# Performance work log

Measured on AMD Instinct MI355X. Metric: run time of the kernel, lower is better.

The kernel has to match this reference:

```python
import jax, jax.numpy as jnp
import numpy as np
import math

HIDDEN = 1024
HEADS = 16
HEAD_DIM = HIDDEN // HEADS
B, S = 2, 2048


def setup_inputs() -> dict:
    key = jax.random.key(0)
    ks = jax.random.split(key, 10)
    std = 1.0 / math.sqrt(HIDDEN)
    mk = lambda k: (jax.random.normal(k, (HIDDEN, HIDDEN), jnp.float32) * std)
    return {
        "hidden_states": jax.random.normal(ks[0], (B, S, HIDDEN), jnp.float32),
        "attention_mask": jnp.zeros((B, 1, 1, S), jnp.float32),
        "wq": mk(ks[1]), "bq": jnp.zeros((HIDDEN,), jnp.float32),
        "wk": mk(ks[2]), "bk": jnp.zeros((HIDDEN,), jnp.float32),
        "wv": mk(ks[3]), "bv": jnp.zeros((HIDDEN,), jnp.float32),
        "wo": mk(ks[4]), "bo": jnp.zeros((HIDDEN,), jnp.float32),
    }


def reference(hidden_states, attention_mask, wq, bq, wk, bk, wv, bv, wo, bo):
    b, s, _ = hidden_states.shape
    scale = math.sqrt(HEAD_DIM)
    # projections (torch Linear: x @ W.T + b); weights stored as [out, in]
    q = hidden_states @ wq.T + bq
    k = hidden_states @ wk.T + bk
    v = hidden_states @ wv.T + bv
    # [B, H, S, D]
    q = q.reshape(b, s, HEADS, HEAD_DIM).transpose(0, 2, 1, 3)
    k = k.reshape(b, s, HEADS, HEAD_DIM).transpose(0, 2, 1, 3)
    v = v.reshape(b, s, HEADS, HEAD_DIM).transpose(0, 2, 1, 3)
    scores = jnp.einsum("bhqd,bhkd->bhqk", q, k) / scale
    scores = scores + attention_mask  # broadcast [B,1,1,S]
    weights = jax.nn.softmax(scores, axis=-1)  # dropout = identity (eval)
    out = jnp.einsum("bhqk,bhkd->bhqd", weights, v)
    out = out.transpose(0, 2, 1, 3).reshape(b, s, HIDDEN)
    out = out @ wo.T + bo
    return out
```

## Files before the change

kernel.cpp:

```cpp
#include <hip/hip_runtime.h>
#include <hip/hip_bf16.h>

typedef __bf16 bf16_t;
typedef __bf16 bf16x8 __attribute__((ext_vector_type(8)));
typedef _Float16 f16x4 __attribute__((ext_vector_type(4)));
typedef _Float16 f16x8 __attribute__((ext_vector_type(8)));
typedef float f32x4 __attribute__((ext_vector_type(4)));

#define SEQ    2048
#define NH     16
#define HD     64
#define HIDDEN 1024
#define LOG2E  1.44269504f

#if __has_builtin(__builtin_amdgcn_exp2f)
#define EXP2F(x) __builtin_amdgcn_exp2f(x)
#else
#define EXP2F(x) exp2f(x)
#endif

__device__ __forceinline__ bf16_t to_bf16(float f) { return (bf16_t)f; }

__device__ __forceinline__ void async16(const void* g, void* l) {
    __builtin_amdgcn_global_load_lds((const __attribute__((address_space(1))) void*)g,
                                     (__attribute__((address_space(3))) void*)l, 16, 0, 0);
}

__global__ __launch_bounds__(256) void cvt_kernel(
    const float* __restrict__ s0, bf16_t* __restrict__ d0, int c0,
    const float* __restrict__ s1, bf16_t* __restrict__ d1, int c1,
    const float* __restrict__ s2, bf16_t* __restrict__ d2, int c2,
    const float* __restrict__ s3, bf16_t* __restrict__ d3, int c3,
    const float* __restrict__ s4, bf16_t* __restrict__ d4, int c4)
{
    int blk = blockIdx.x;
    const float* s; bf16_t* d;
    if (blk < c0)              { s = s0; d = d0; }
    else if ((blk -= c0) < c1) { s = s1; d = d1; }
    else if ((blk -= c1) < c2) { s = s2; d = d2; }
    else if ((blk -= c2) < c3) { s = s3; d = d3; }
    else                       { blk -= c3; s = s4; d = d4; }
    const size_t base = (size_t)blk * 2048 + threadIdx.x * 8;
    const float4 a = *(const float4*)&s[base];
    const float4 b = *(const float4*)&s[base + 4];
    bf16x8 o;
    o[0] = (bf16_t)a.x; o[1] = (bf16_t)a.y; o[2] = (bf16_t)a.z; o[3] = (bf16_t)a.w;
    o[4] = (bf16_t)b.x; o[5] = (bf16_t)b.y; o[6] = (bf16_t)b.z; o[7] = (bf16_t)b.w;
    *(bf16x8*)&d[base] = o;
}

__global__ __launch_bounds__(256, 3) void qkv_kernel(
    const bf16_t* __restrict__ X,
    const bf16_t* __restrict__ wq, const bf16_t* __restrict__ wk, const bf16_t* __restrict__ wv,
    const float* __restrict__ bq, const float* __restrict__ bk, const float* __restrict__ bv,
    bf16_t* __restrict__ qws, bf16_t* __restrict__ kws, _Float16* __restrict__ vws)
{
    __shared__ __align__(16) bf16_t Sh[16384];
    const int z = blockIdx.z;
    const bf16_t* Wsel = (z == 0) ? wq : (z == 1) ? wk : wv;
    const float*  bsel = (z == 0) ? bq : (z == 1) ? bk : bv;
    const int m0 = blockIdx.y * 128, n0 = blockIdx.x * 128;

    const int t = threadIdx.x, lane = t & 63, w = t >> 6;
    const int w0 = w & 1, w1 = w >> 1, l15 = lane & 15, q4 = lane >> 4;

    f32x4 acc[4][4];
#pragma unroll
    for (int i = 0; i < 4; i++)
#pragma unroll
        for (int j = 0; j < 4; j++) acc[i][j] = f32x4{0.f, 0.f, 0.f, 0.f};

    auto stage = [&](int kt, int buf) {
#pragma unroll
        for (int j = 0; j < 2; j++) {
            const int s = j * 256 + t;
            const int row = s >> 2, c = (s & 3) ^ (row & 3);
            const int lb = buf * 8192 + (j * 256 + w * 64) * 8;
            async16(&X[(size_t)(m0 + row) * HIDDEN + kt + c * 8], &Sh[lb]);
            async16(&Wsel[(size_t)(n0 + row) * HIDDEN + kt + c * 8], &Sh[lb + 4096]);
        }
    };
    stage(0, 0);

    for (int it = 0; it < 32; it++) {
        const int cur = it & 1;
        __syncthreads();
        if (it < 31) stage((it + 1) * 32, cur ^ 1);
        const bf16_t* As = &Sh[cur * 8192];
        const bf16_t* Bs = &Sh[cur * 8192 + 4096];
        bf16x8 af[4];
#pragma unroll
        for (int ti = 0; ti < 4; ti++) {
            const int ra = w0 * 64 + ti * 16 + l15;
            af[ti] = *(const bf16x8*)&As[ra * 32 + (q4 ^ (ra & 3)) * 8];
        }
#pragma unroll
        for (int tj = 0; tj < 4; tj++) {
            const int rb = w1 * 64 + tj * 16 + l15;
            const bf16x8 bfr = *(const bf16x8*)&Bs[rb * 32 + (q4 ^ (rb & 3)) * 8];
#pragma unroll
            for (int ti = 0; ti < 4; ti++)
                acc[ti][tj] = __builtin_amdgcn_mfma_f32_16x16x32_bf16(af[ti], bfr, acc[ti][tj], 0, 0, 0);
        }
    }
    __syncthreads();

    if (z < 2) {
#pragma unroll
        for (int tj = 0; tj < 4; tj++) {
            const int n = w1 * 64 + tj * 16 + l15;
            const float bb = bsel[n0 + n];
            const int ch = (n >> 3), sub = n & 7;
#pragma unroll
            for (int ti = 0; ti < 4; ti++)
#pragma unroll
                for (int r = 0; r < 4; r++) {
                    const int m = w0 * 64 + ti * 16 + q4 * 4 + r;
                    Sh[m * 128 + ((ch ^ (m & 15)) << 3) + sub] = to_bf16(acc[ti][tj][r] + bb);
                }
        }
        __syncthreads();
        bf16_t* dst = (z == 0) ? qws : kws;
#pragma unroll
        for (int i = 0; i < 8; i++) {
            const int g = i * 256 + t;
            const int row = g >> 4, c = g & 15;
            const bf16x8 vv = *(const bf16x8*)&Sh[row * 128 + ((c ^ (row & 15)) << 3)];
            *(bf16x8*)&dst[(size_t)(m0 + row) * HIDDEN + n0 + c * 8] = vv;
        }
    } else {
        _Float16* Vt = (_Float16*)Sh;
#pragma unroll
        for (int tj = 0; tj < 4; tj++) {
            const int n = w1 * 64 + tj * 16 + l15;
            const float bb = bsel[n0 + n];
#pragma unroll
            for (int ti = 0; ti < 4; ti++) {
                const int mb = w0 * 64 + ti * 16 + q4 * 4;
                f16x4 v;
#pragma unroll
                for (int r = 0; r < 4; r++) v[r] = (_Float16)(acc[ti][tj][r] + bb);
                *(f16x4*)&Vt[n * 128 + (((mb >> 3) ^ (n & 15)) << 3) + (mb & 7)] = v;
            }
        }
        __syncthreads();
        const int b = m0 >> 11, sbase = m0 & (SEQ - 1);
#pragma unroll
        for (int i = 0; i < 8; i++) {
            const int g = i * 256 + t;
            const int row = g >> 4, c = g & 15;
            const f16x8 vv = *(const f16x8*)&Vt[row * 128 + ((c ^ (row & 15)) << 3)];
            const int d = (n0 + row) & 63, hh = (n0 + row) >> 6;
            *(f16x8*)&vws[(((size_t)b * NH + hh) * HD + d) * SEQ + sbase + c * 8] = vv;
        }
    }
}

__global__ __launch_bounds__(256, 4) void attn_kernel(
    const bf16_t* __restrict__ Qw, const bf16_t* __restrict__ Kw,
    const _Float16* __restrict__ Vtw, const float* __restrict__ Mask,
    bf16_t* __restrict__ Ow)
{
    __shared__ __align__(16) bf16_t Tiles[2][2][64 * 64];

    const int t = threadIdx.x, lane = t & 63, w = t >> 6;
    const int l15 = lane & 15, q4 = lane >> 4;
    const int lid = blockIdx.x;
    const int c8 = lid & 7, jx = lid >> 3;
    const int bh = c8 * 4 + (jx >> 5);
    const int q0 = (jx & 31) * 64;
    const int b = bh >> 4, h = bh & 15;

    const bf16_t* Qh = Qw + (size_t)b * SEQ * HIDDEN + h * HD;
    const bf16_t* Kh = Kw + (size_t)b * SEQ * HIDDEN + h * HD;
    const _Float16* Vh = Vtw + (size_t)bh * HD * SEQ;
    const float* Mrow = Mask + (size_t)b * SEQ;

    const int qrow = q0 + w * 16 + l15;
    bf16x8 qf[2];
#pragma unroll
    for (int ks = 0; ks < 2; ks++)
        qf[ks] = *(const bf16x8*)&Qh[(size_t)qrow * HIDDEN + ks * 32 + q4 * 8];

    f32x4 oacc[4];
#pragma unroll
    for (int nb = 0; nb < 4; nb++) oacc[nb] = f32x4{0.f, 0.f, 0.f, 0.f};
    float psum = 0.f;

    auto stageKV = [&](int ti, int buf) {
        const int kt = ti * 64;
        bf16_t*   Kd = &Tiles[buf][0][0];
        _Float16* Vd = (_Float16*)&Tiles[buf][1][0];
#pragma unroll
        for (int g = 0; g < 2; g++) {
            const int s = g * 256 + t;
            const int row = s >> 3, c = (s & 7) ^ (row & 7);
            const int lbase = (g * 256 + w * 64) * 8;
            async16(&Kh[(size_t)(kt + row) * HIDDEN + c * 8], &Kd[lbase]);
            async16(&Vh[(size_t)row * SEQ + kt + c * 8], &Vd[lbase]);
        }
    };

    stageKV(0, 0);

    for (int it = 0; it < 32; it++) {
        const int cur = it & 1;
        __syncthreads();
        if (it < 31) stageKV(it + 1, cur ^ 1);

        const int kt = it * 64;
        const bf16_t*   Ksh = &Tiles[cur][0][0];
        const _Float16* Vsh = (const _Float16*)&Tiles[cur][1][0];

        float4 mv4[4];
#pragma unroll
        for (int cb = 0; cb < 4; cb++) mv4[cb] = *(const float4*)&Mrow[kt + cb * 16 + q4 * 4];

        f32x4 sa[4];
#pragma unroll
        for (int cb = 0; cb < 4; cb++) sa[cb] = f32x4{0.f, 0.f, 0.f, 0.f};
#pragma unroll
        for (int cb = 0; cb < 4; cb++) {
            const int rk = cb * 16 + l15;
#pragma unroll
            for (int ks = 0; ks < 2; ks++) {
                const bf16x8 kf = *(const bf16x8*)&Ksh[rk * 64 + (((ks * 4 + q4) ^ (rk & 7))) * 8];
                sa[cb] = __builtin_amdgcn_mfma_f32_16x16x32_bf16(kf, qf[ks], sa[cb], 0, 0, 0);
            }
        }

        f16x8 pa[2];
#pragma unroll
        for (int cb = 0; cb < 4; cb++) {
            const float4 mv = mv4[cb];
            const float mk[4] = {mv.x * LOG2E, mv.y * LOG2E, mv.z * LOG2E, mv.w * LOG2E};
#pragma unroll
            for (int r = 0; r < 4; r++) {
                const float p = EXP2F(fmaf(sa[cb][r], 0.125f * LOG2E, mk[r]));
                psum += p;
                pa[cb >> 1][(cb & 1) * 4 + r] = (_Float16)p;
            }
        }

#pragma unroll
        for (int t2 = 0; t2 < 2; t2++) {
#pragma unroll
            for (int nb = 0; nb < 4; nb++) {
                const int rv = nb * 16 + l15;
                const int glo = (t2 * 4 + (q4 >> 1)) ^ (rv & 7);
                const int ghi = (t2 * 4 + 2 + (q4 >> 1)) ^ (rv & 7);
                const f16x4 vlo = *(const f16x4*)&Vsh[rv * 64 + (glo << 3) + (q4 & 1) * 4];
                const f16x4 vhi = *(const f16x4*)&Vsh[rv * 64 + (ghi << 3) + (q4 & 1) * 4];
                f16x8 vf;
                vf[0] = vlo[0]; vf[1] = vlo[1]; vf[2] = vlo[2]; vf[3] = vlo[3];
                vf[4] = vhi[0]; vf[5] = vhi[1]; vf[6] = vhi[2]; vf[7] = vhi[3];
                oacc[nb] = __builtin_amdgcn_mfma_f32_16x16x32_f16(pa[t2], vf, oacc[nb], 0, 0, 0);
            }
        }
    }

    psum += __shfl_xor(psum, 16);
    psum += __shfl_xor(psum, 32);

    float inv[4];
#pragma unroll
    for (int r = 0; r < 4; r++) inv[r] = 1.f / __shfl(psum, q4 * 4 + r);
#pragma unroll
    for (int r = 0; r < 4; r++) {
        const int srow = q0 + w * 16 + q4 * 4 + r;
#pragma unroll
        for (int nb = 0; nb < 4; nb++)
            Ow[((size_t)b * SEQ + srow) * HIDDEN + h * HD + nb * 16 + l15] =
                to_bf16(oacc[nb][r] * inv[r]);
    }
}

__global__ __launch_bounds__(256, 2) void oproj_kernel(
    const bf16_t* __restrict__ A, const bf16_t* __restrict__ Wo,
    const float* __restrict__ bo, float* __restrict__ Out)
{
    __shared__ __align__(16) bf16_t Sh[12288];
    const int m0 = blockIdx.y * 64, n0 = blockIdx.x * 128;
    const int t = threadIdx.x, lane = t & 63, w = t >> 6;
    const int l15 = lane & 15, q4 = lane >> 4;

    f32x4 acc[4][2];
#pragma unroll
    for (int i = 0; i < 4; i++)
#pragma unroll
        for (int j = 0; j < 2; j++) acc[i][j] = f32x4{0.f, 0.f, 0.f, 0.f};

    auto stage = [&](int kt, int buf) {
        {
            const int row = t >> 2, c = (t & 3) ^ (row & 3);
            async16(&A[(size_t)(m0 + row) * HIDDEN + kt + c * 8], &Sh[buf * 6144 + w * 64 * 8]);
        }
#pragma unroll
        for (int j = 0; j < 2; j++) {
            const int s = j * 256 + t;
            const int row = s >> 2, c = (s & 3) ^ (row & 3);
            async16(&Wo[(size_t)(n0 + row) * HIDDEN + kt + c * 8],
                    &Sh[buf * 6144 + 2048 + (j * 256 + w * 64) * 8]);
        }
    };
    stage(0, 0);

    for (int it = 0; it < 32; it++) {
        const int cur = it & 1;
        __syncthreads();
        if (it < 31) stage((it + 1) * 32, cur ^ 1);
        const bf16_t* As = &Sh[cur * 6144];
        const bf16_t* Bs = &Sh[cur * 6144 + 2048];
        bf16x8 af[4];
#pragma unroll
        for (int ti = 0; ti < 4; ti++) {
            const int ra = ti * 16 + l15;
            af[ti] = *(const bf16x8*)&As[ra * 32 + (q4 ^ (ra & 3)) * 8];
        }
#pragma unroll
        for (int tj = 0; tj < 2; tj++) {
            const int rb = w * 32 + tj * 16 + l15;
            const bf16x8 bfr = *(const bf16x8*)&Bs[rb * 32 + (q4 ^ (rb & 3)) * 8];
#pragma unroll
            for (int ti = 0; ti < 4; ti++)
                acc[ti][tj] = __builtin_amdgcn_mfma_f32_16x16x32_bf16(bfr, af[ti], acc[ti][tj], 0, 0, 0);
        }
    }

#pragma unroll
    for (int tj = 0; tj < 2; tj++) {
        const int nb4 = n0 + w * 32 + tj * 16 + q4 * 4;
        const float4 bb = *(const float4*)&bo[nb4];
#pragma unroll
        for (int ti = 0; ti < 4; ti++) {
            const int m = m0 + ti * 16 + l15;
            float4 ov;
            ov.x = acc[ti][tj][0] + bb.x;
            ov.y = acc[ti][tj][1] + bb.y;
            ov.z = acc[ti][tj][2] + bb.z;
            ov.w = acc[ti][tj][3] + bb.w;
            *(float4*)&Out[(size_t)m * HIDDEN + nb4] = ov;
        }
    }
}

extern "C" void kernel_launch(void* const* d_in, const int* in_sizes, int n_in,
                              void* d_out, int out_size, void* d_ws, size_t ws_size,
                              hipStream_t stream) {
    const float* X   = (const float*)d_in[0];
    const float* msk = (const float*)d_in[1];
    const float* wq  = (const float*)d_in[2];
    const float* bq  = (const float*)d_in[3];
    const float* wk  = (const float*)d_in[4];
    const float* bk  = (const float*)d_in[5];
    const float* wv  = (const float*)d_in[6];
    const float* bv  = (const float*)d_in[7];
    const float* wo  = (const float*)d_in[8];
    const float* bo  = (const float*)d_in[9];
    float* out = (float*)d_out;

    const size_t NELT = (size_t)2 * SEQ * HIDDEN;
    const size_t WELT = (size_t)HIDDEN * HIDDEN;
    bf16_t*    xbf = (bf16_t*)d_ws;
    bf16_t*    qws = xbf + NELT;
    bf16_t*    kws = qws + NELT;
    _Float16*  vws = (_Float16*)(kws + NELT);
    bf16_t*    aws = xbf;
    bf16_t*    wqb = (bf16_t*)d_out;
    bf16_t*    wkb = wqb + WELT;
    bf16_t*    wvb = wkb + WELT;
    bf16_t*    wob = wvb + WELT;

    cvt_kernel<<<dim3(2048 + 4 * 512), dim3(256), 0, stream>>>(
        X, xbf, 2048, wq, wqb, 512, wk, wkb, 512, wv, wvb, 512, wo, wob, 512);
    qkv_kernel<<<dim3(8, 32, 3), dim3(256), 0, stream>>>(
        xbf, wqb, wkb, wvb, bq, bk, bv, qws, kws, vws);
    attn_kernel<<<dim3(1024), dim3(256), 0, stream>>>(qws, kws, vws, msk, aws);
    oproj_kernel<<<dim3(8, 64), dim3(256), 0, stream>>>(aws, wob, bo, out);
}
```

Baseline: 200.1 us.

## Pre-permute V layout for single-load fragments, prescale mask, precompute LDS offsets

Stores V in the workspace in a permuted key order, so each attention lane can fetch its V MFMA fragment with one 8-wide LDS load instead of two 4-wide loads plus a repack. Premultiplies the mask by log2(e) in the conversion kernel, precomputes the swizzled LDS offsets and global staging pointers, and unrolls the main loop by two so buffer indices are constant. A pairwise reduction of psum shortens the dependency chain. The aim is fewer LDS instructions and less address and ALU work in the inner loop, in exchange for a more intricate V layout and a small extra mask workspace placed after the bf16 weights in the output buffer.

```diff
diff --git a/kernel.cpp b/kernel.cpp
--- a/kernel.cpp
+++ b/kernel.cpp
@@ -31,7 +31,8 @@
     const float* __restrict__ s1, bf16_t* __restrict__ d1, int c1,
     const float* __restrict__ s2, bf16_t* __restrict__ d2, int c2,
     const float* __restrict__ s3, bf16_t* __restrict__ d3, int c3,
-    const float* __restrict__ s4, bf16_t* __restrict__ d4, int c4)
+    const float* __restrict__ s4, bf16_t* __restrict__ d4, int c4,
+    const float* __restrict__ s5, float* __restrict__ d5)
 {
     int blk = blockIdx.x;
     const float* s; bf16_t* d;
@@ -39,7 +40,18 @@
     else if ((blk -= c0) < c1) { s = s1; d = d1; }
     else if ((blk -= c1) < c2) { s = s2; d = d2; }
     else if ((blk -= c2) < c3) { s = s3; d = d3; }
-    else                       { blk -= c3; s = s4; d = d4; }
+    else if ((blk -= c3) < c4) { s = s4; d = d4; }
+    else {
+        blk -= c4;
+        const size_t base = (size_t)blk * 2048 + threadIdx.x * 8;
+        float4 a = *(const float4*)&s5[base];
+        float4 b = *(const float4*)&s5[base + 4];
+        a.x *= LOG2E; a.y *= LOG2E; a.z *= LOG2E; a.w *= LOG2E;
+        b.x *= LOG2E; b.y *= LOG2E; b.z *= LOG2E; b.w *= LOG2E;
+        *(float4*)&d5[base] = a;
+        *(float4*)&d5[base + 4] = b;
+        return;
+    }
     const size_t base = (size_t)blk * 2048 + threadIdx.x * 8;
     const float4 a = *(const float4*)&s[base];
     const float4 b = *(const float4*)&s[base + 4];
@@ -149,7 +161,13 @@
         for (int i = 0; i < 8; i++) {
             const int g = i * 256 + t;
             const int row = g >> 4, c = g & 15;
-            const f16x8 vv = *(const f16x8*)&Vt[row * 128 + ((c ^ (row & 15)) << 3)];
+            const int sA = (c >> 2) * 32 + (c & 3) * 4;
+            const int sB = sA + 16;
+            const f16x4 va = *(const f16x4*)&Vt[row * 128 + (((sA >> 3) ^ (row & 15)) << 3) + (sA & 7)];
+            const f16x4 vb = *(const f16x4*)&Vt[row * 128 + (((sB >> 3) ^ (row & 15)) << 3) + (sB & 7)];
+            f16x8 vv;
+            vv[0] = va[0]; vv[1] = va[1]; vv[2] = va[2]; vv[3] = va[3];
+            vv[4] = vb[0]; vv[5] = vb[1]; vv[6] = vb[2]; vv[7] = vb[3];
             const int d = (n0 + row) & 63, hh = (n0 + row) >> 6;
             *(f16x8*)&vws[(((size_t)b * NH + hh) * HD + d) * SEQ + sbase + c * 8] = vv;
         }
@@ -158,7 +176,7 @@
 
 __global__ __launch_bounds__(256, 4) void attn_kernel(
     const bf16_t* __restrict__ Qw, const bf16_t* __restrict__ Kw,
-    const _Float16* __restrict__ Vtw, const float* __restrict__ Mask,
+    const _Float16* __restrict__ Vtw, const float* __restrict__ Msc,
     bf16_t* __restrict__ Ow)
 {
     __shared__ __align__(16) bf16_t Tiles[2][2][64 * 64];
@@ -174,7 +192,7 @@
     const bf16_t* Qh = Qw + (size_t)b * SEQ * HIDDEN + h * HD;
     const bf16_t* Kh = Kw + (size_t)b * SEQ * HIDDEN + h * HD;
     const _Float16* Vh = Vtw + (size_t)bh * HD * SEQ;
-    const float* Mrow = Mask + (size_t)b * SEQ;
+    const float* Mrow = Msc + (size_t)b * SEQ;
 
     const int qrow = q0 + w * 16 + l15;
     bf16x8 qf[2];
@@ -187,76 +205,91 @@
     for (int nb = 0; nb < 4; nb++) oacc[nb] = f32x4{0.f, 0.f, 0.f, 0.f};
     float psum = 0.f;
 
-    auto stageKV = [&](int ti, int buf) {
-        const int kt = ti * 64;
+    int koff[8];
+#pragma unroll
+    for (int cb = 0; cb < 4; cb++)
+#pragma unroll
+        for (int ks = 0; ks < 2; ks++) {
+            const int rk = cb * 16 + l15;
+            koff[cb * 2 + ks] = rk * 64 + (((ks * 4 + q4) ^ (rk & 7)) << 3);
+        }
+    int voff[8];
+#pragma unroll
+    for (int t2 = 0; t2 < 2; t2++)
+#pragma unroll
+        for (int nb = 0; nb < 4; nb++) {
+            const int rv = nb * 16 + l15;
+            voff[t2 * 4 + nb] = rv * 64 + (((t2 * 4 + q4) ^ (rv & 7)) << 3);
+        }
+
+    const int rs0 = t >> 3, cs0 = (t & 7) ^ (rs0 & 7);
+    const int rs1 = 32 + rs0, cs1 = (t & 7) ^ (rs1 & 7);
+    const bf16_t*   Kp0 = Kh + (size_t)rs0 * HIDDEN + cs0 * 8;
+    const bf16_t*   Kp1 = Kh + (size_t)rs1 * HIDDEN + cs1 * 8;
+    const _Float16* Vp0 = Vh + (size_t)rs0 * SEQ + cs0 * 8;
+    const _Float16* Vp1 = Vh + (size_t)rs1 * SEQ + cs1 * 8;
+    const int db0 = (0 * 256 + w * 64) * 8, db1 = (1 * 256 + w * 64) * 8;
+
+    auto stageKV = [&](int it, int buf) {
+        const int kt = it * 64;
         bf16_t*   Kd = &Tiles[buf][0][0];
         _Float16* Vd = (_Float16*)&Tiles[buf][1][0];
-#pragma unroll
-        for (int g = 0; g < 2; g++) {
-            const int s = g * 256 + t;
-            const int row = s >> 3, c = (s & 7) ^ (row & 7);
-            const int lbase = (g * 256 + w * 64) * 8;
-            async16(&Kh[(size_t)(kt + row) * HIDDEN + c * 8], &Kd[lbase]);
-            async16(&Vh[(size_t)row * SEQ + kt + c * 8], &Vd[lbase]);
-        }
+        async16(Kp0 + (size_t)kt * HIDDEN, &Kd[db0]);
+        async16(Vp0 + kt,                  &Vd[db0]);
+        async16(Kp1 + (size_t)kt * HIDDEN, &Kd[db1]);
+        async16(Vp1 + kt,                  &Vd[db1]);
     };
 
-    stageKV(0, 0);
-
-    for (int it = 0; it < 32; it++) {
-        const int cur = it & 1;
+    auto iterBody = [&](int it, int buf) {
         __syncthreads();
-        if (it < 31) stageKV(it + 1, cur ^ 1);
-
-        const int kt = it * 64;
-        const bf16_t*   Ksh = &Tiles[cur][0][0];
-        const _Float16* Vsh = (const _Float16*)&Tiles[cur][1][0];
+        if (it < 31) stageKV(it + 1, buf ^ 1);
+
+        const bf16_t*   Ksh = &Tiles[buf][0][0];
+        const _Float16* Vsh = (const _Float16*)&Tiles[buf][1][0];
 
         float4 mv4[4];
 #pragma unroll
-        for (int cb = 0; cb < 4; cb++) mv4[cb] = *(const float4*)&Mrow[kt + cb * 16 + q4 * 4];
+        for (int cb = 0; cb < 4; cb++) mv4[cb] = *(const float4*)&Mrow[it * 64 + cb * 16 + q4 * 4];
 
         f32x4 sa[4];
 #pragma unroll
         for (int cb = 0; cb < 4; cb++) sa[cb] = f32x4{0.f, 0.f, 0.f, 0.f};
 #pragma unroll
-        for (int cb = 0; cb < 4; cb++) {
-            const int rk = cb * 16 + l15;
+        for (int cb = 0; cb < 4; cb++)
 #pragma unroll
             for (int ks = 0; ks < 2; ks++) {
-                const bf16x8 kf = *(const bf16x8*)&Ksh[rk * 64 + (((ks * 4 + q4) ^ (rk & 7))) * 8];
+                const bf16x8 kf = *(const bf16x8*)&Ksh[koff[cb * 2 + ks]];
                 sa[cb] = __builtin_amdgcn_mfma_f32_16x16x32_bf16(kf, qf[ks], sa[cb], 0, 0, 0);
             }
-        }
 
         f16x8 pa[2];
 #pragma unroll
         for (int cb = 0; cb < 4; cb++) {
             const float4 mv = mv4[cb];
-            const float mk[4] = {mv.x * LOG2E, mv.y * LOG2E, mv.z * LOG2E, mv.w * LOG2E};
+            const float mk[4] = {mv.x, mv.y, mv.z, mv.w};
+            float p[4];
 #pragma unroll
             for (int r = 0; r < 4; r++) {
-                const float p = EXP2F(fmaf(sa[cb][r], 0.125f * LOG2E, mk[r]));
-                psum += p;
-                pa[cb >> 1][(cb & 1) * 4 + r] = (_Float16)p;
+                p[r] = EXP2F(fmaf(sa[cb][r], 0.125f * LOG2E, mk[r]));
+                pa[cb >> 1][(cb & 1) * 4 + r] = (_Float16)p[r];
             }
-        }
-
-#pragma unroll
-        for (int t2 = 0; t2 < 2; t2++) {
+            psum += (p[0] + p[1]) + (p[2] + p[3]);
+        }
+
+#pragma unroll
+        for (int t2 = 0; t2 < 2; t2++)
 #pragma unroll
             for (int nb = 0; nb < 4; nb++) {
-                const int rv = nb * 16 + l15;
-                const int glo = (t2 * 4 + (q4 >> 1)) ^ (rv & 7);
-                const int ghi = (t2 * 4 + 2 + (q4 >> 1)) ^ (rv & 7);
-                const f16x4 vlo = *(const f16x4*)&Vsh[rv * 64 + (glo << 3) + (q4 & 1) * 4];
-                const f16x4 vhi = *(const f16x4*)&Vsh[rv * 64 + (ghi << 3) + (q4 & 1) * 4];
-                f16x8 vf;
-                vf[0] = vlo[0]; vf[1] = vlo[1]; vf[2] = vlo[2]; vf[3] = vlo[3];
-                vf[4] = vhi[0]; vf[5] = vhi[1]; vf[6] = vhi[2]; vf[7] = vhi[3];
+                const f16x8 vf = *(const f16x8*)&Vsh[voff[t2 * 4 + nb]];
                 oacc[nb] = __builtin_amdgcn_mfma_f32_16x16x32_f16(pa[t2], vf, oacc[nb], 0, 0, 0);
             }
-        }
+    };
+
+    stageKV(0, 0);
+#pragma unroll 1
+    for (int it2 = 0; it2 < 16; it2++) {
+        iterBody(it2 * 2, 0);
+        iterBody(it2 * 2 + 1, 1);
     }
 
     psum += __shfl_xor(psum, 16);
@@ -370,11 +403,13 @@
     bf16_t*    wkb = wqb + WELT;
     bf16_t*    wvb = wkb + WELT;
     bf16_t*    wob = wvb + WELT;
-
-    cvt_kernel<<<dim3(2048 + 4 * 512), dim3(256), 0, stream>>>(
-        X, xbf, 2048, wq, wqb, 512, wk, wkb, 512, wv, wvb, 512, wo, wob, 512);
+    float*     mws = (float*)(wob + WELT);
+
+    cvt_kernel<<<dim3(2048 + 4 * 512 + 2), dim3(256), 0, stream>>>(
+        X, xbf, 2048, wq, wqb, 512, wk, wkb, 512, wv, wvb, 512, wo, wob, 512,
+        msk, mws);
     qkv_kernel<<<dim3(8, 32, 3), dim3(256), 0, stream>>>(
         xbf, wqb, wkb, wvb, bq, bk, bv, qws, kws, vws);
-    attn_kernel<<<dim3(1024), dim3(256), 0, stream>>>(qws, kws, vws, msk, aws);
+    attn_kernel<<<dim3(1024), dim3(256), 0, stream>>>(qws, kws, vws, mws, aws);
     oproj_kernel<<<dim3(8, 64), dim3(256), 0, stream>>>(aws, wob, bo, out);
 }
```

Result: faster. 192.8 us (-3.7%).
